# Performance work log

Measured on AMD Instinct MI355X. Metric: run time of the kernel, lower is better.

The kernel has to match this reference:

```python
import jax, jax.numpy as jnp
import numpy as np

B, S, D, H = 4, 2048, 1024, 16
DK = D // H


def setup_inputs() -> dict:
    key = jax.random.key(0)
    ks = jax.random.split(key, 12)
    s = 1.0 / np.sqrt(D)
    inp = {
        "q": jax.random.normal(ks[0], (B, S, D), jnp.float32),
        "k": jax.random.normal(ks[1], (B, S, D), jnp.float32),
        "v": jax.random.normal(ks[2], (B, S, D), jnp.float32),
        # causal mask, broadcastable over batch and heads
        "mask": jnp.tril(jnp.ones((S, S), jnp.int32))[None, None, :, :],
        "Wq": jax.random.uniform(ks[3], (D, D), jnp.float32, -s, s),
        "bq": jax.random.uniform(ks[4], (D,), jnp.float32, -s, s),
        "Wk": jax.random.uniform(ks[5], (D, D), jnp.float32, -s, s),
        "bk": jax.random.uniform(ks[6], (D,), jnp.float32, -s, s),
        "Wv": jax.random.uniform(ks[7], (D, D), jnp.float32, -s, s),
        "bv": jax.random.uniform(ks[8], (D,), jnp.float32, -s, s),
        "Wo": jax.random.uniform(ks[9], (D, D), jnp.float32, -s, s),
        "bo": jax.random.uniform(ks[10], (D,), jnp.float32, -s, s),
    }
    return inp


def reference(q, k, v, mask, Wq, bq, Wk, bk, Wv, bv, Wo, bo):
    def split_heads(x):  # [B,S,D] -> [B,H,S,DK]
        return x.reshape(B, S, H, DK).transpose(0, 2, 1, 3)

    qh = split_heads(q @ Wq.T + bq)
    kh = split_heads(k @ Wk.T + bk)
    vh = split_heads(v @ Wv.T + bv)

    scores = jnp.einsum("bhqd,bhkd->bhqk", qh, kh) / jnp.sqrt(jnp.float32(DK))
    scores = jnp.where(mask == 0, jnp.float32(-1e9), scores)
    attn = jax.nn.softmax(scores, axis=-1)
    out = jnp.einsum("bhqk,bhkd->bhqd", attn, vh)
    out = out.transpose(0, 2, 1, 3).reshape(B, S, D)
    return out @ Wo.T + bo
```

## Files before the change

kernel.cpp:

```cpp
#include <hip/hip_runtime.h>
#include <cstdint>

#define Bb 4
#define Ss 2048
#define Dd 1024
#define Hh 16

typedef unsigned short u16;
typedef unsigned int u32;
typedef __attribute__((ext_vector_type(8))) short short8;
typedef __attribute__((ext_vector_type(8))) _Float16 half8;
typedef __attribute__((ext_vector_type(2))) __fp16 fp16x2;
typedef __attribute__((ext_vector_type(4))) float floatx4;
typedef __attribute__((ext_vector_type(16))) float floatx16;
typedef __attribute__((address_space(3))) u32 lds_u32;
typedef const __attribute__((address_space(1))) u32 glob_u32;

__device__ __forceinline__ u16 f2bf(float x) {
  union { float f; u32 u; } v; v.f = x;
  u32 r = v.u + 0x7fffu + ((v.u >> 16) & 1u);
  return (u16)(r >> 16);
}

__device__ __forceinline__ u32 pk2(float a, float b) {
  union { fp16x2 h; u32 u; } cv;
  cv.h = __builtin_amdgcn_cvt_pkrtz(a, b);
  return cv.u;
}

__device__ __forceinline__ half8 h8_from(u32 a, u32 b, u32 c, u32 d) {
  union { u32 u[4]; half8 h; } t;
  t.u[0] = a; t.u[1] = b; t.u[2] = c; t.u[3] = d;
  return t.h;
}

__global__ __launch_bounds__(256) void cvt_many(const float* __restrict__ s0,
                                                const float* __restrict__ s1,
                                                const float* __restrict__ s2,
                                                const float* __restrict__ s3,
                                                u16* __restrict__ d0,
                                                u16* __restrict__ d1,
                                                u16* __restrict__ d2,
                                                u16* __restrict__ d3, int n8) {
  int z = blockIdx.y;
  const float* s = z == 0 ? s0 : z == 1 ? s1 : z == 2 ? s2 : s3;
  u16* d = z == 0 ? d0 : z == 1 ? d1 : z == 2 ? d2 : d3;
  int i = blockIdx.x * 256 + threadIdx.x;
  if (i >= n8) return;
  const float4* sp = (const float4*)s;
  float4 a = sp[2 * i], b = sp[2 * i + 1];
  u32 w0 = (u32)f2bf(a.x) | ((u32)f2bf(a.y) << 16);
  u32 w1 = (u32)f2bf(a.z) | ((u32)f2bf(a.w) << 16);
  u32 w2 = (u32)f2bf(b.x) | ((u32)f2bf(b.y) << 16);
  u32 w3 = (u32)f2bf(b.z) | ((u32)f2bf(b.w) << 16);
  ((uint4*)d)[i] = make_uint4(w0, w1, w2, w3);
}

template <int MODE>
__device__ __forceinline__ void gemm_body(const u16* __restrict__ A,
                                          const u16* __restrict__ Bw,
                                          const float* __restrict__ bias,
                                          void* __restrict__ Cout, float scale) {
  __shared__ u16 As[128 * 64];
  __shared__ u16 Bs[128 * 64];
  int tid = threadIdx.x;
  int wave = tid >> 6, lane = tid & 63;
  int quad = lane >> 4, l16 = lane & 15;
  int m0 = blockIdx.x * 128, n0 = blockIdx.y * 128;
  int wr = (wave >> 1) * 64, wc = (wave & 1) * 64;
  int s7 = l16 & 7;
  int srow = wave * 8 + (lane >> 3);
  int gcol = (((lane & 7) ^ (lane >> 3)) << 3);

  floatx4 vzero = {0.f, 0.f, 0.f, 0.f};
  floatx4 acc[4][4];
#pragma unroll
  for (int i = 0; i < 4; ++i)
#pragma unroll
    for (int j = 0; j < 4; ++j) acc[i][j] = vzero;

  for (int kt = 0; kt < Dd; kt += 64) {
    __syncthreads();
#pragma unroll
    for (int c = 0; c < 4; ++c) {
      int r = c * 32 + srow;
      __builtin_amdgcn_global_load_lds(
          (glob_u32*)&A[(size_t)(m0 + r) * Dd + kt + gcol],
          (lds_u32*)&As[(c * 32 + wave * 8) * 64], 16, 0, 0);
      __builtin_amdgcn_global_load_lds(
          (glob_u32*)&Bw[(size_t)(n0 + r) * Dd + kt + gcol],
          (lds_u32*)&Bs[(c * 32 + wave * 8) * 64], 16, 0, 0);
    }
    __syncthreads();
#pragma unroll
    for (int kk = 0; kk < 2; ++kk) {
      short8 af[4], bf[4];
#pragma unroll
      for (int i = 0; i < 4; ++i)
        af[i] = *(const short8*)&As[(wr + i * 16 + l16) * 64 + (((quad + 4 * kk) ^ s7) << 3)];
#pragma unroll
      for (int j = 0; j < 4; ++j)
        bf[j] = *(const short8*)&Bs[(wc + j * 16 + l16) * 64 + (((quad + 4 * kk) ^ s7) << 3)];
#pragma unroll
      for (int i = 0; i < 4; ++i)
#pragma unroll
        for (int j = 0; j < 4; ++j)
          acc[i][j] = __builtin_amdgcn_mfma_f32_16x16x32_bf16(af[i], bf[j], acc[i][j], 0, 0, 0);
    }
  }

#pragma unroll
  for (int i = 0; i < 4; ++i) {
#pragma unroll
    for (int j = 0; j < 4; ++j) {
#pragma unroll
      for (int r = 0; r < 4; ++r) {
        int m = m0 + wr + i * 16 + quad * 4 + r;
        int n = n0 + wc + j * 16 + l16;
        float val = (acc[i][j][r] + bias[n]) * scale;
        if (MODE == 0) {
          int b = m >> 11, s = m & (Ss - 1);
          int h = n >> 6, dk = n & 63;
          ((u16*)Cout)[((((size_t)b * Hh + h) * Ss + s) << 6) + dk] = f2bf(val);
        } else {
          ((float*)Cout)[(size_t)m * Dd + n] = val;
        }
      }
    }
  }
}

__global__ __launch_bounds__(256) void gemm_qkv(const u16* qb, const u16* kb, const u16* vb,
                                                const u16* Wq, const u16* Wk, const u16* Wv,
                                                const float* bq, const float* bk, const float* bv,
                                                u16* qo, u16* ko, u16* vo) {
  const float K1 = 0.18033688f;
  int z = blockIdx.z;
  const u16* A = z == 0 ? qb : z == 1 ? kb : vb;
  const u16* W = z == 0 ? Wq : z == 1 ? Wk : Wv;
  const float* bi = z == 0 ? bq : z == 1 ? bk : bv;
  u16* o = z == 0 ? qo : z == 1 ? ko : vo;
  gemm_body<0>(A, W, bi, o, z == 0 ? K1 : 1.0f);
}

__global__ __launch_bounds__(256) void gemm_out(const u16* A, const u16* W,
                                                const float* bi, float* o) {
  gemm_body<1>(A, W, bi, o, 1.0f);
}

__global__ __launch_bounds__(256) void transpose_v(const u16* __restrict__ in,
                                                   _Float16* __restrict__ out) {
  __shared__ u16 T[64 * 72];
  int bh = blockIdx.y, s0 = blockIdx.x * 64, tid = threadIdx.x;
#pragma unroll
  for (int c = 0; c < 2; ++c) {
    int e = c * 2048 + tid * 8;
    int r = e >> 6, col = e & 63;
    *(uint4*)&T[r * 72 + col] = *(const uint4*)&in[((size_t)bh * Ss + s0 + r) * 64 + col];
  }
  __syncthreads();
#pragma unroll
  for (int c = 0; c < 2; ++c) {
    int e = c * 2048 + tid * 8;
    int d = e >> 6, sc = e & 63;
    _Float16 tmp[8];
#pragma unroll
    for (int j = 0; j < 8; ++j) {
      union { u32 u; float f; } cv;
      cv.u = (u32)T[(sc + j) * 72 + d] << 16;
      tmp[j] = (_Float16)cv.f;
    }
    *(uint4*)&out[((size_t)bh * 64 + d) * Ss + s0 + sc] = *(uint4*)tmp;
  }
}

#define MFIX 4.0f
#define SW(a, b) asm("v_permlane32_swap_b32 %0, %1" : "+v"(a), "+v"(b))
#define VRD(CH, NT) \
  (*(const half8*)&Vt[p][((NT) * 32 + l31) * 64 + ((((CH) + hi) ^ s7b) << 3)])

#define TILE_BODY(NST, MASKED)                                                \
  do {                                                                        \
    short8 kf0[4], kf1[4];                                                    \
    _Pragma("unroll") for (int m = 0; m < 4; ++m) {                           \
      kf0[m] = *(const short8*)&Kt[p][l31 * 64 + (((2 * m + hi) ^ s7b) << 3)];\
      if (NST == 2)                                                           \
        kf1[m] = *(const short8*)&Kt[p][(32 + l31) * 64 +                     \
                                        (((2 * m + hi) ^ s7b) << 3)];         \
    }                                                                         \
    floatx16 sc0, sc1;                                                        \
    _Pragma("unroll") for (int r = 0; r < 16; ++r) {                          \
      sc0[r] = -MFIX;                                                         \
      sc1[r] = -MFIX;                                                         \
    }                                                                         \
    __builtin_amdgcn_s_setprio(1);                                            \
    _Pragma("unroll") for (int m = 0; m < 4; ++m) {                           \
      sc0 = __builtin_amdgcn_mfma_f32_32x32x16_bf16(kf0[m], qf[m], sc0, 0, 0, 0); \
      if (NST == 2)                                                           \
        sc1 = __builtin_amdgcn_mfma_f32_32x32x16_bf16(kf1[m], qf[m], sc1, 0, 0, 0); \
    }                                                                         \
    __builtin_amdgcn_s_setprio(0);                                            \
    if (MASKED) {                                                             \
      int qrow = Rq + l31;                                                    \
      _Pragma("unroll") for (int r = 0; r < 16; ++r) {                        \
        int key = k0 + 4 * hi + (r & 3) + 8 * (r >> 2);                       \
        if (key > qrow) sc0[r] = -3e38f;                                      \
        if (NST == 2 && key + 32 > qrow) sc1[r] = -3e38f;                     \
      }                                                                       \
    }                                                                         \
    u32 c0[8], c1[8];                                                         \
    float rs = 0.f;                                                           \
    _Pragma("unroll") for (int j = 0; j < 8; ++j) {                           \
      float p0 = __builtin_amdgcn_exp2f(sc0[2 * j]);                          \
      float p1 = __builtin_amdgcn_exp2f(sc0[2 * j + 1]);                      \
      rs += p0 + p1;                                                          \
      c0[j] = pk2(p0, p1);                                                    \
      if (NST == 2) {                                                         \
        float p2 = __builtin_amdgcn_exp2f(sc1[2 * j]);                        \
        float p3 = __builtin_amdgcn_exp2f(sc1[2 * j + 1]);                    \
        rs += p2 + p3;                                                        \
        c1[j] = pk2(p2, p3);                                                  \
      }                                                                       \
    }                                                                         \
    l_part += rs;                                                             \
    SW(c0[0], c0[2]); SW(c0[1], c0[3]); SW(c0[4], c0[6]); SW(c0[5], c0[7]);   \
    if (NST == 2) {                                                           \
      SW(c1[0], c1[2]); SW(c1[1], c1[3]); SW(c1[4], c1[6]); SW(c1[5], c1[7]); \
    }                                                                         \
    __builtin_amdgcn_s_setprio(1);                                            \
    {                                                                         \
      half8 pa = h8_from(c0[0], c0[1], c0[2], c0[3]);                         \
      o0 = __builtin_amdgcn_mfma_f32_32x32x16_f16(pa, VRD(0, 0), o0, 0, 0, 0);\
      o1 = __builtin_amdgcn_mfma_f32_32x32x16_f16(pa, VRD(0, 1), o1, 0, 0, 0);\
      half8 pb = h8_from(c0[4], c0[5], c0[6], c0[7]);                         \
      o0 = __builtin_amdgcn_mfma_f32_32x32x16_f16(pb, VRD(2, 0), o0, 0, 0, 0);\
      o1 = __builtin_amdgcn_mfma_f32_32x32x16_f16(pb, VRD(2, 1), o1, 0, 0, 0);\
      if (NST == 2) {                                                         \
        half8 pc = h8_from(c1[0], c1[1], c1[2], c1[3]);                       \
        o0 = __builtin_amdgcn_mfma_f32_32x32x16_f16(pc, VRD(4, 0), o0, 0, 0, 0); \
        o1 = __builtin_amdgcn_mfma_f32_32x32x16_f16(pc, VRD(4, 1), o1, 0, 0, 0); \
        half8 pd = h8_from(c1[4], c1[5], c1[6], c1[7]);                       \
        o0 = __builtin_amdgcn_mfma_f32_32x32x16_f16(pd, VRD(6, 0), o0, 0, 0, 0); \
        o1 = __builtin_amdgcn_mfma_f32_32x32x16_f16(pd, VRD(6, 1), o1, 0, 0, 0); \
      }                                                                       \
    }                                                                         \
    __builtin_amdgcn_s_setprio(0);                                            \
  } while (0)

__global__ __launch_bounds__(256) void attn_kernel(const u16* __restrict__ qh,
                                                   const u16* __restrict__ kh,
                                                   const _Float16* __restrict__ vT,
                                                   u16* __restrict__ ctx) {
  __shared__ u16 Kt[2][64 * 64];
  __shared__ _Float16 Vt[2][64 * 64];

  int tid = threadIdx.x, w = tid >> 6, lane = tid & 63;
  int hi = lane >> 5, l31 = lane & 31, s7b = lane & 7;
  int bh = blockIdx.x;
  int sp = blockIdx.y;
  const u16* Q = qh + (size_t)bh * Ss * 64;
  const u16* K = kh + (size_t)bh * Ss * 64;
  const _Float16* V = vT + (size_t)bh * 64 * Ss;

  int Rq = (w < 2) ? 64 * sp + 32 * w : 64 * (31 - sp) + 32 * (w - 2);

  short8 qf[4];
#pragma unroll
  for (int m = 0; m < 4; ++m)
    qf[m] = *(const short8*)&Q[(size_t)(Rq + l31) * 64 + m * 16 + hi * 8];

  floatx16 o0, o1;
#pragma unroll
  for (int r = 0; r < 16; ++r) { o0[r] = 0.f; o1[r] = 0.f; }
  float l_part = 0.f;

  int lrow = w * 8 + (lane >> 3);
  int g8 = ((lane & 7) ^ (lane >> 3)) << 3;
  int nkt = 32 - sp;

#define STAGE(P, KT)                                                          \
  do {                                                                        \
    int _k0 = (KT) * 64;                                                      \
    __builtin_amdgcn_global_load_lds(                                         \
        (glob_u32*)&K[(size_t)(_k0 + lrow) * 64 + g8],                        \
        (lds_u32*)&Kt[P][w * 512], 16, 0, 0);                                 \
    __builtin_amdgcn_global_load_lds(                                         \
        (glob_u32*)&K[(size_t)(_k0 + 32 + lrow) * 64 + g8],                   \
        (lds_u32*)&Kt[P][2048 + w * 512], 16, 0, 0);                          \
    __builtin_amdgcn_global_load_lds(                                         \
        (glob_u32*)&V[(size_t)lrow * Ss + _k0 + g8],                          \
        (lds_u32*)&Vt[P][w * 512], 16, 0, 0);                                 \
    __builtin_amdgcn_global_load_lds(                                         \
        (glob_u32*)&V[(size_t)(32 + lrow) * Ss + _k0 + g8],                   \
        (lds_u32*)&Vt[P][2048 + w * 512], 16, 0, 0);                          \
  } while (0)

  STAGE(0, 0);

  int p = 0;
  for (int kt = 0; kt < nkt; ++kt) {
    int k0 = kt * 64;
    __syncthreads();
    if (kt + 1 < nkt) STAGE(p ^ 1, kt + 1);

    if (k0 + 63 <= Rq) {
      TILE_BODY(2, false);
    } else if (k0 <= Rq + 31) {
      if (k0 + 32 <= Rq + 31) TILE_BODY(2, true);
      else TILE_BODY(1, true);
    }
    p ^= 1;
  }
#undef STAGE

  float l2 = l_part + __shfl_xor(l_part, 32, 64);
  float linv = 1.0f / l2;
  int b = bh >> 4, h = bh & 15;
#pragma unroll
  for (int r = 0; r < 16; ++r) {
    int qi = (r & 3) + 8 * (r >> 2) + 4 * hi;
    float li = __shfl(linv, qi, 64);
    size_t base = ((size_t)b * Ss + Rq + qi) * Dd + h * 64 + l31;
    ctx[base] = f2bf(o0[r] * li);
    ctx[base + 32] = f2bf(o1[r] * li);
  }
}

extern "C" void kernel_launch(void* const* d_in, const int* in_sizes, int n_in,
                              void* d_out, int out_size, void* d_ws, size_t ws_size,
                              hipStream_t stream) {
  const float* q = (const float*)d_in[0];
  const float* k = (const float*)d_in[1];
  const float* v = (const float*)d_in[2];
  const float* Wq = (const float*)d_in[4];
  const float* bq = (const float*)d_in[5];
  const float* Wk = (const float*)d_in[6];
  const float* bk = (const float*)d_in[7];
  const float* Wv = (const float*)d_in[8];
  const float* bv = (const float*)d_in[9];
  const float* Wo = (const float*)d_in[10];
  const float* bo = (const float*)d_in[11];

  char* ws = (char*)d_ws;
  const size_t MB = 1024 * 1024;
  u16* qb = (u16*)(ws + 0 * MB);
  u16* kb = (u16*)(ws + 16 * MB);
  u16* vb = (u16*)(ws + 32 * MB);
  u16* Wqb = (u16*)(ws + 48 * MB);
  u16* Wkb = (u16*)(ws + 50 * MB);
  u16* Wvb = (u16*)(ws + 52 * MB);
  u16* Wob = (u16*)(ws + 54 * MB);
  u16* qhp = (u16*)(ws + 56 * MB);
  u16* khp = (u16*)(ws + 72 * MB);
  u16* vhp = (u16*)(ws + 88 * MB);
  _Float16* vhT = (_Float16*)kb;
  u16* ctx = qb;

  const int nQKV8 = (Bb * Ss * Dd) / 8;
  const int nW8 = (Dd * Dd) / 8;
  {
    dim3 g(nQKV8 / 256, 3);
    cvt_many<<<g, 256, 0, stream>>>(q, k, v, v, qb, kb, vb, vb, nQKV8);
  }
  {
    dim3 g(nW8 / 256, 4);
    cvt_many<<<g, 256, 0, stream>>>(Wq, Wk, Wv, Wo, Wqb, Wkb, Wvb, Wob, nW8);
  }
  {
    dim3 g((Bb * Ss) / 128, Dd / 128, 3);
    gemm_qkv<<<g, 256, 0, stream>>>(qb, kb, vb, Wqb, Wkb, Wvb, bq, bk, bv, qhp, khp, vhp);
  }
  {
    dim3 g(Ss / 64, Bb * Hh);
    transpose_v<<<g, 256, 0, stream>>>(vhp, vhT);
  }
  {
    dim3 g(Bb * Hh, 16);
    attn_kernel<<<g, 256, 0, stream>>>(qhp, khp, vhT, ctx);
  }
  {
    dim3 g((Bb * Ss) / 128, Dd / 128);
    gemm_out<<<g, 256, 0, stream>>>(ctx, Wob, bo, (float*)d_out);
  }
}
```

Baseline: 335.3 us.

## Fuse V transpose into QKV GEMM, merge conversions, reshape attention to 2-wave blocks

The V projection epilogue now writes fp16 directly in transposed layout, which removes the separate transpose kernel and the bf16 round trip. The two float-to-bf16 conversion launches are merged into one launch with seven slices. The attention kernel changes from 256-thread blocks that pair a light and a heavy query tile to 128-thread blocks, each owning one 64-row query tile, launched heaviest first. This costs some load balancing within a block and relies on the scheduler to spread the uneven causal work across blocks.

```diff
diff --git a/kernel.cpp b/kernel.cpp
--- a/kernel.cpp
+++ b/kernel.cpp
@@ -34,17 +34,19 @@
   return t.h;
 }
 
-__global__ __launch_bounds__(256) void cvt_many(const float* __restrict__ s0,
-                                                const float* __restrict__ s1,
-                                                const float* __restrict__ s2,
-                                                const float* __restrict__ s3,
-                                                u16* __restrict__ d0,
-                                                u16* __restrict__ d1,
-                                                u16* __restrict__ d2,
-                                                u16* __restrict__ d3, int n8) {
+__global__ __launch_bounds__(256) void cvt_many(
+    const float* __restrict__ s0, const float* __restrict__ s1,
+    const float* __restrict__ s2, const float* __restrict__ s3,
+    const float* __restrict__ s4, const float* __restrict__ s5,
+    const float* __restrict__ s6, u16* __restrict__ d0, u16* __restrict__ d1,
+    u16* __restrict__ d2, u16* __restrict__ d3, u16* __restrict__ d4,
+    u16* __restrict__ d5, u16* __restrict__ d6, int nA, int nW) {
   int z = blockIdx.y;
-  const float* s = z == 0 ? s0 : z == 1 ? s1 : z == 2 ? s2 : s3;
-  u16* d = z == 0 ? d0 : z == 1 ? d1 : z == 2 ? d2 : d3;
+  const float* s = z == 0 ? s0 : z == 1 ? s1 : z == 2 ? s2
+                   : z == 3 ? s3 : z == 4 ? s4 : z == 5 ? s5 : s6;
+  u16* d = z == 0 ? d0 : z == 1 ? d1 : z == 2 ? d2
+           : z == 3 ? d3 : z == 4 ? d4 : z == 5 ? d5 : d6;
+  int n8 = z < 3 ? nA : nW;
   int i = blockIdx.x * 256 + threadIdx.x;
   if (i >= n8) return;
   const float4* sp = (const float4*)s;
@@ -60,7 +62,8 @@
 __device__ __forceinline__ void gemm_body(const u16* __restrict__ A,
                                           const u16* __restrict__ Bw,
                                           const float* __restrict__ bias,
-                                          void* __restrict__ Cout, float scale) {
+                                          void* __restrict__ Cout, float scale,
+                                          int vtrans) {
   __shared__ u16 As[128 * 64];
   __shared__ u16 Bs[128 * 64];
   int tid = threadIdx.x;
@@ -113,17 +116,28 @@
   for (int i = 0; i < 4; ++i) {
 #pragma unroll
     for (int j = 0; j < 4; ++j) {
-#pragma unroll
-      for (int r = 0; r < 4; ++r) {
-        int m = m0 + wr + i * 16 + quad * 4 + r;
-        int n = n0 + wc + j * 16 + l16;
-        float val = (acc[i][j][r] + bias[n]) * scale;
-        if (MODE == 0) {
-          int b = m >> 11, s = m & (Ss - 1);
-          int h = n >> 6, dk = n & 63;
-          ((u16*)Cout)[((((size_t)b * Hh + h) * Ss + s) << 6) + dk] = f2bf(val);
-        } else {
-          ((float*)Cout)[(size_t)m * Dd + n] = val;
+      int n = n0 + wc + j * 16 + l16;
+      if (MODE == 0 && vtrans) {
+        int h = n >> 6, dk = n & 63;
+        int b = m0 >> 11;
+        int sb = (m0 + wr + i * 16 + quad * 4) & (Ss - 1);
+        union { _Float16 h4[4]; uint2 u2; } pv;
+#pragma unroll
+        for (int r = 0; r < 4; ++r)
+          pv.h4[r] = (_Float16)((acc[i][j][r] + bias[n]) * scale);
+        *(uint2*)&((_Float16*)Cout)[((size_t)(b * Hh + h) * 64 + dk) * Ss + sb] = pv.u2;
+      } else {
+#pragma unroll
+        for (int r = 0; r < 4; ++r) {
+          int m = m0 + wr + i * 16 + quad * 4 + r;
+          float val = (acc[i][j][r] + bias[n]) * scale;
+          if (MODE == 0) {
+            int b = m >> 11, s = m & (Ss - 1);
+            int h = n >> 6, dk = n & 63;
+            ((u16*)Cout)[((((size_t)b * Hh + h) * Ss + s) << 6) + dk] = f2bf(val);
+          } else {
+            ((float*)Cout)[(size_t)m * Dd + n] = val;
+          }
         }
       }
     }
@@ -133,45 +147,19 @@
 __global__ __launch_bounds__(256) void gemm_qkv(const u16* qb, const u16* kb, const u16* vb,
                                                 const u16* Wq, const u16* Wk, const u16* Wv,
                                                 const float* bq, const float* bk, const float* bv,
-                                                u16* qo, u16* ko, u16* vo) {
+                                                u16* qo, u16* ko, _Float16* vT) {
   const float K1 = 0.18033688f;
   int z = blockIdx.z;
   const u16* A = z == 0 ? qb : z == 1 ? kb : vb;
   const u16* W = z == 0 ? Wq : z == 1 ? Wk : Wv;
   const float* bi = z == 0 ? bq : z == 1 ? bk : bv;
-  u16* o = z == 0 ? qo : z == 1 ? ko : vo;
-  gemm_body<0>(A, W, bi, o, z == 0 ? K1 : 1.0f);
+  void* o = z == 0 ? (void*)qo : z == 1 ? (void*)ko : (void*)vT;
+  gemm_body<0>(A, W, bi, o, z == 0 ? K1 : 1.0f, z == 2);
 }
 
 __global__ __launch_bounds__(256) void gemm_out(const u16* A, const u16* W,
                                                 const float* bi, float* o) {
-  gemm_body<1>(A, W, bi, o, 1.0f);
-}
-
-__global__ __launch_bounds__(256) void transpose_v(const u16* __restrict__ in,
-                                                   _Float16* __restrict__ out) {
-  __shared__ u16 T[64 * 72];
-  int bh = blockIdx.y, s0 = blockIdx.x * 64, tid = threadIdx.x;
-#pragma unroll
-  for (int c = 0; c < 2; ++c) {
-    int e = c * 2048 + tid * 8;
-    int r = e >> 6, col = e & 63;
-    *(uint4*)&T[r * 72 + col] = *(const uint4*)&in[((size_t)bh * Ss + s0 + r) * 64 + col];
-  }
-  __syncthreads();
-#pragma unroll
-  for (int c = 0; c < 2; ++c) {
-    int e = c * 2048 + tid * 8;
-    int d = e >> 6, sc = e & 63;
-    _Float16 tmp[8];
-#pragma unroll
-    for (int j = 0; j < 8; ++j) {
-      union { u32 u; float f; } cv;
-      cv.u = (u32)T[(sc + j) * 72 + d] << 16;
-      tmp[j] = (_Float16)cv.f;
-    }
-    *(uint4*)&out[((size_t)bh * 64 + d) * Ss + s0 + sc] = *(uint4*)tmp;
-  }
+  gemm_body<1>(A, W, bi, o, 1.0f, 0);
 }
 
 #define MFIX 4.0f
@@ -247,7 +235,7 @@
     __builtin_amdgcn_s_setprio(0);                                            \
   } while (0)
 
-__global__ __launch_bounds__(256) void attn_kernel(const u16* __restrict__ qh,
+__global__ __launch_bounds__(128) void attn_kernel(const u16* __restrict__ qh,
                                                    const u16* __restrict__ kh,
                                                    const _Float16* __restrict__ vT,
                                                    u16* __restrict__ ctx) {
@@ -257,12 +245,12 @@
   int tid = threadIdx.x, w = tid >> 6, lane = tid & 63;
   int hi = lane >> 5, l31 = lane & 31, s7b = lane & 7;
   int bh = blockIdx.x;
-  int sp = blockIdx.y;
+  int s = 31 - blockIdx.y;
   const u16* Q = qh + (size_t)bh * Ss * 64;
   const u16* K = kh + (size_t)bh * Ss * 64;
   const _Float16* V = vT + (size_t)bh * 64 * Ss;
 
-  int Rq = (w < 2) ? 64 * sp + 32 * w : 64 * (31 - sp) + 32 * (w - 2);
+  int Rq = 64 * s + 32 * w;
 
   short8 qf[4];
 #pragma unroll
@@ -274,40 +262,37 @@
   for (int r = 0; r < 16; ++r) { o0[r] = 0.f; o1[r] = 0.f; }
   float l_part = 0.f;
 
-  int lrow = w * 8 + (lane >> 3);
-  int g8 = ((lane & 7) ^ (lane >> 3)) << 3;
-  int nkt = 32 - sp;
+  int srow = tid >> 3;
+  int g8 = ((tid & 7) ^ ((tid >> 3) & 7)) << 3;
 
 #define STAGE(P, KT)                                                          \
   do {                                                                        \
     int _k0 = (KT) * 64;                                                      \
-    __builtin_amdgcn_global_load_lds(                                         \
-        (glob_u32*)&K[(size_t)(_k0 + lrow) * 64 + g8],                        \
-        (lds_u32*)&Kt[P][w * 512], 16, 0, 0);                                 \
-    __builtin_amdgcn_global_load_lds(                                         \
-        (glob_u32*)&K[(size_t)(_k0 + 32 + lrow) * 64 + g8],                   \
-        (lds_u32*)&Kt[P][2048 + w * 512], 16, 0, 0);                          \
-    __builtin_amdgcn_global_load_lds(                                         \
-        (glob_u32*)&V[(size_t)lrow * Ss + _k0 + g8],                          \
-        (lds_u32*)&Vt[P][w * 512], 16, 0, 0);                                 \
-    __builtin_amdgcn_global_load_lds(                                         \
-        (glob_u32*)&V[(size_t)(32 + lrow) * Ss + _k0 + g8],                   \
-        (lds_u32*)&Vt[P][2048 + w * 512], 16, 0, 0);                          \
+    _Pragma("unroll") for (int c = 0; c < 4; ++c) {                           \
+      int r_ = c * 16 + srow;                                                 \
+      __builtin_amdgcn_global_load_lds(                                       \
+          (glob_u32*)&K[(size_t)(_k0 + r_) * 64 + g8],                        \
+          (lds_u32*)&Kt[P][(c * 16 + w * 8) * 64], 16, 0, 0);                 \
+      __builtin_amdgcn_global_load_lds(                                       \
+          (glob_u32*)&V[(size_t)r_ * Ss + _k0 + g8],                          \
+          (lds_u32*)&Vt[P][(c * 16 + w * 8) * 64], 16, 0, 0);                 \
+    }                                                                         \
   } while (0)
 
   STAGE(0, 0);
 
   int p = 0;
-  for (int kt = 0; kt < nkt; ++kt) {
+  for (int kt = 0; kt <= s; ++kt) {
     int k0 = kt * 64;
     __syncthreads();
-    if (kt + 1 < nkt) STAGE(p ^ 1, kt + 1);
-
-    if (k0 + 63 <= Rq) {
+    if (kt < s) STAGE(p ^ 1, kt + 1);
+
+    if (kt < s) {
       TILE_BODY(2, false);
-    } else if (k0 <= Rq + 31) {
-      if (k0 + 32 <= Rq + 31) TILE_BODY(2, true);
-      else TILE_BODY(1, true);
+    } else if (w == 0) {
+      TILE_BODY(1, true);
+    } else {
+      TILE_BODY(2, true);
     }
     p ^= 1;
   }
@@ -352,31 +337,23 @@
   u16* Wob = (u16*)(ws + 54 * MB);
   u16* qhp = (u16*)(ws + 56 * MB);
   u16* khp = (u16*)(ws + 72 * MB);
-  u16* vhp = (u16*)(ws + 88 * MB);
-  _Float16* vhT = (_Float16*)kb;
+  _Float16* vhT = (_Float16*)(ws + 88 * MB);
   u16* ctx = qb;
 
-  const int nQKV8 = (Bb * Ss * Dd) / 8;
+  const int nA8 = (Bb * Ss * Dd) / 8;
   const int nW8 = (Dd * Dd) / 8;
   {
-    dim3 g(nQKV8 / 256, 3);
-    cvt_many<<<g, 256, 0, stream>>>(q, k, v, v, qb, kb, vb, vb, nQKV8);
-  }
-  {
-    dim3 g(nW8 / 256, 4);
-    cvt_many<<<g, 256, 0, stream>>>(Wq, Wk, Wv, Wo, Wqb, Wkb, Wvb, Wob, nW8);
+    dim3 g(nA8 / 256, 7);
+    cvt_many<<<g, 256, 0, stream>>>(q, k, v, Wq, Wk, Wv, Wo,
+                                    qb, kb, vb, Wqb, Wkb, Wvb, Wob, nA8, nW8);
   }
   {
     dim3 g((Bb * Ss) / 128, Dd / 128, 3);
-    gemm_qkv<<<g, 256, 0, stream>>>(qb, kb, vb, Wqb, Wkb, Wvb, bq, bk, bv, qhp, khp, vhp);
+    gemm_qkv<<<g, 256, 0, stream>>>(qb, kb, vb, Wqb, Wkb, Wvb, bq, bk, bv, qhp, khp, vhT);
   }
   {
-    dim3 g(Ss / 64, Bb * Hh);
-    transpose_v<<<g, 256, 0, stream>>>(vhp, vhT);
-  }
-  {
-    dim3 g(Bb * Hh, 16);
-    attn_kernel<<<g, 256, 0, stream>>>(qhp, khp, vhT, ctx);
+    dim3 g(Bb * Hh, 32);
+    attn_kernel<<<g, 128, 0, stream>>>(qhp, khp, vhT, ctx);
   }
   {
     dim3 g((Bb * Ss) / 128, Dd / 128);
```

Measured after the change: 324.8 us. 1.03x faster.
